# Kernel optimization log

Measured on AMD Instinct MI355X. Metric: run time of the kernel, lower is better.

The kernel has to match this reference:

```python
import jax, jax.numpy as jnp
import numpy as np

B = 8192
D_IN = 512
D_HID = 256
D_OUT = 128
EPS_STD = 1e-5
EPS_NORM = 1e-12


def _embed(x, W1, b1, W2, b2):
    # head: Linear -> ReLU -> Linear
    h = jax.nn.relu(x @ W1 + b1)          # (b, 256)
    y = h @ W2 + b2                        # (b, 128)
    # white(): per-feature batch whitening (center + unit std, unbiased like torch.std)
    mu = jnp.mean(y, axis=0, keepdims=True)
    sd = jnp.std(y, axis=0, keepdims=True, ddof=1) + EPS_STD
    y = (y - mu) / sd
    # F.normalize(p=2, dim=1)
    n = jnp.maximum(jnp.linalg.norm(y, axis=1, keepdims=True), EPS_NORM)
    return y / n


def _pair_loss(v1, v2):
    b = v1.shape[0]
    cat = jnp.concatenate([v1, v2], axis=0)            # (2b, d)
    inner = v1 @ cat.T                                  # (b, 2b) == broadcasted (v1*cat).sum(2)
    mask = jnp.concatenate(
        [1.0 - jnp.eye(b, dtype=inner.dtype), jnp.ones((b, b), dtype=inner.dtype)], axis=1)
    logits = inner * mask                               # zero out self-similarity logits
    logp = jax.nn.log_softmax(logits, axis=1)
    tgt = jnp.arange(b, 2 * b)                          # positive = matching row in v2 block
    return -jnp.take_along_axis(logp, tgt[:, None], axis=1).mean()


def setup_inputs() -> dict:
    key = jax.random.key(0)
    ks = jax.random.split(key, 16)
    def lin_init(k, fin, fout):
        bound = 1.0 / np.sqrt(fin)
        kw, kb = jax.random.split(k)
        W = jax.random.uniform(kw, (fin, fout), jnp.float32, -bound, bound)
        b = jax.random.uniform(kb, (fout,), jnp.float32, -bound, bound)
        return W, b
    inp = {
        'x_B': jax.random.normal(ks[0], (B, D_IN), jnp.float32),
        'x_E': jax.random.normal(ks[1], (B, D_IN), jnp.float32),
        'x_F': jax.random.normal(ks[2], (B, D_IN), jnp.float32),
    }
    for i, m in enumerate('BEF'):
        W1, b1 = lin_init(ks[3 + 2 * i], D_IN, D_HID)
        W2, b2 = lin_init(ks[4 + 2 * i], D_HID, D_OUT)
        inp[f'W1_{m}'] = W1; inp[f'b1_{m}'] = b1
        inp[f'W2_{m}'] = W2; inp[f'b2_{m}'] = b2
    return inp


def reference(x_B, x_E, x_F,
              W1_B, b1_B, W2_B, b2_B,
              W1_E, b1_E, W2_E, b2_E,
              W1_F, b1_F, W2_F, b2_F):
    zB = _embed(x_B, W1_B, b1_B, W2_B, b2_B)
    zE = _embed(x_E, W1_E, b1_E, W2_E, b2_E)
    zF = _embed(x_F, W1_F, b1_F, W2_F, b2_F)
    pairs = [(zB, zE), (zB, zF), (zE, zF)]  # itertools.combinations order
    loss = sum(_pair_loss(v1, v2) for v1, v2 in pairs) / len(pairs)
    return loss
```

## Files before the change

kernel.cpp:

```cpp
#include <hip/hip_runtime.h>
#include <hip/hip_bf16.h>
#include <math.h>

#define NROWS 8192
#define DIN   512
#define DHID  256
#define DOUT  128
#define LOG2E 1.4426950408889634f

typedef unsigned short ushort_t;
typedef __attribute__((ext_vector_type(8))) short bf16x8;
typedef __attribute__((ext_vector_type(4))) float f32x4;

#if defined(__has_builtin)
#  if __has_builtin(__builtin_amdgcn_exp2f)
#    define FAST_EXP2(x) __builtin_amdgcn_exp2f(x)
#  else
#    define FAST_EXP2(x) exp2f(x)
#  endif
#else
#  define FAST_EXP2(x) exp2f(x)
#endif

__device__ __forceinline__ short f2bf(float x) {
  __hip_bfloat16 h = __float2bfloat16(x);
  return *(short*)&h;
}

__device__ __forceinline__ bf16x8 cvt8(float4 lo, float4 hi) {
  bf16x8 r;
  r[0] = f2bf(lo.x); r[1] = f2bf(lo.y); r[2] = f2bf(lo.z); r[3] = f2bf(lo.w);
  r[4] = f2bf(hi.x); r[5] = f2bf(hi.y); r[6] = f2bf(hi.z); r[7] = f2bf(hi.w);
  return r;
}

__device__ __forceinline__ void dma16(const void* g, void* l) {
  __builtin_amdgcn_global_load_lds(
      (const __attribute__((address_space(1))) unsigned int*)g,
      (__attribute__((address_space(3))) unsigned int*)l, 16, 0, 0);
}

__global__ __launch_bounds__(256) void prep_w_kernel(
    const float* __restrict__ W1_0, const float* __restrict__ W1_1,
    const float* __restrict__ W1_2,
    const float* __restrict__ W2_0, const float* __restrict__ W2_1,
    const float* __restrict__ W2_2,
    ushort_t* __restrict__ w1t3, ushort_t* __restrict__ w2t3,
    float* __restrict__ zero_region)
{
  const int z = blockIdx.y;
  if (z == 0 && blockIdx.x < 163)
    zero_region[blockIdx.x * 256 + threadIdx.x] = 0.0f;
  const float* W1 = z == 0 ? W1_0 : (z == 1 ? W1_1 : W1_2);
  const float* W2 = z == 0 ? W2_0 : (z == 1 ? W2_1 : W2_2);
  int idx = blockIdx.x * 256 + threadIdx.x;
  if (idx < DHID * DIN) {
    int n = idx >> 9, k = idx & (DIN - 1);
    w1t3[(size_t)z * DHID * DIN + idx] = f2bf(W1[(size_t)k * DHID + n]);
  } else {
    int j = idx - DHID * DIN;
    int n = j >> 8, k = j & (DHID - 1);
    w2t3[(size_t)z * DOUT * DHID + j] = f2bf(W2[(size_t)k * DOUT + n]);
  }
}

#define MLP_BUF 20480
__global__ __launch_bounds__(256, 3) void mlp_kernel(
    const float* __restrict__ x0, const float* __restrict__ x1,
    const float* __restrict__ x2,
    const ushort_t* __restrict__ w1t3,
    const float* __restrict__ b1_0, const float* __restrict__ b1_1,
    const float* __restrict__ b1_2,
    const ushort_t* __restrict__ w2t3,
    const float* __restrict__ b2_0, const float* __restrict__ b2_1,
    const float* __restrict__ b2_2,
    float* __restrict__ y3,
    float* __restrict__ colsum, float* __restrict__ colsumsq)
{
  const int z = blockIdx.y;
  const float* X  = z == 0 ? x0 : (z == 1 ? x1 : x2);
  const float* B1 = z == 0 ? b1_0 : (z == 1 ? b1_1 : b1_2);
  const float* B2 = z == 0 ? b2_0 : (z == 1 ? b2_1 : b2_2);
  const ushort_t* W1t = w1t3 + (size_t)z * DHID * DIN;
  const ushort_t* W2t = w2t3 + (size_t)z * DOUT * DHID;
  float* Y    = y3 + (size_t)z * NROWS * DOUT;
  float* csum = colsum + z * DOUT;
  float* csq  = colsumsq + z * DOUT;

  __shared__ __align__(16) char lds[2 * MLP_BUF];
  ushort_t* hs = (ushort_t*)lds;

  const int tid = threadIdx.x, lane = tid & 63, wave = tid >> 6;
  const int quad = lane >> 4, l16 = lane & 15;
  const int m0 = blockIdx.x * 32;

  const char* w1b = (const char*)W1t;
  const char* wsrc[4];
#pragma unroll
  for (int jj = 0; jj < 4; jj++)
    wsrc[jj] = w1b + (size_t)(16 * (wave * 4 + jj) + l16) * 1024 +
               (lane >> 4) * 16;
  const int row8 = lane >> 3, slot = lane & 7;
  const int gseg = (slot + row8) & 7;
  const char* xsrc = (const char*)X +
      (size_t)(m0 + 8 * wave + row8) * 2048 + gseg * 16;

  f32x4 acc1[2][4] = {};
#pragma unroll
  for (int jj = 0; jj < 4; jj++)
    dma16(wsrc[jj], lds + (wave * 4 + jj) * 1024);
  dma16(xsrc, lds + 16384 + wave * 1024);
  __syncthreads();

  for (int c = 0; c < 16; c++) {
    const int buf = c & 1;
    if (c + 1 < 16) {
      char* dst = lds + (buf ^ 1) * MLP_BUF;
#pragma unroll
      for (int jj = 0; jj < 4; jj++)
        dma16(wsrc[jj] + (c + 1) * 64, dst + (wave * 4 + jj) * 1024);
      dma16(xsrc + (c + 1) * 128, dst + 16384 + wave * 1024);
    }
    const char* wb = lds + buf * MLP_BUF;
    const char* xb = wb + 16384;
    bf16x8 a[2];
#pragma unroll
    for (int mt = 0; mt < 2; mt++) {
      const int r = mt * 16 + l16, r7 = r & 7;
      const int s0 = (2 * quad - r7) & 7, s1 = (2 * quad + 1 - r7) & 7;
      float4 v0 = *(const float4*)(xb + r * 128 + s0 * 16);
      float4 v1 = *(const float4*)(xb + r * 128 + s1 * 16);
      a[mt] = cvt8(v0, v1);
    }
    bf16x8 b[4];
#pragma unroll
    for (int ct = 0; ct < 4; ct++)
      b[ct] = *(const bf16x8*)(wb + (wave * 4 + ct) * 1024 + quad * 256 +
                               l16 * 16);
#pragma unroll
    for (int mt = 0; mt < 2; mt++)
#pragma unroll
      for (int ct = 0; ct < 4; ct++)
        acc1[mt][ct] = __builtin_amdgcn_mfma_f32_16x16x32_bf16(
            a[mt], b[ct], acc1[mt][ct], 0, 0, 0);
    __syncthreads();
  }

  bf16x8 b2f[2][8];
#pragma unroll
  for (int ct = 0; ct < 2; ct++)
#pragma unroll
    for (int kk = 0; kk < 8; kk++)
      b2f[ct][kk] = *(const bf16x8*)(W2t +
          (size_t)(wave * 32 + ct * 16 + l16) * DHID + kk * 32 + quad * 8);

#pragma unroll
  for (int ct = 0; ct < 4; ct++) {
    float bb = B1[wave * 64 + ct * 16 + l16];
#pragma unroll
    for (int mt = 0; mt < 2; mt++)
#pragma unroll
      for (int reg = 0; reg < 4; reg++) {
        float v = fmaxf(acc1[mt][ct][reg] + bb, 0.0f);
        hs[(mt * 16 + quad * 4 + reg) * 264 + wave * 64 + ct * 16 + l16] =
            (ushort_t)f2bf(v);
      }
  }
  __syncthreads();

  f32x4 acc2[2][2] = {};
#pragma unroll
  for (int kk = 0; kk < 8; kk++) {
    bf16x8 a2[2];
#pragma unroll
    for (int mt = 0; mt < 2; mt++)
      a2[mt] = *(const bf16x8*)(hs + (mt * 16 + l16) * 264 + kk * 32 +
                                quad * 8);
#pragma unroll
    for (int mt = 0; mt < 2; mt++)
#pragma unroll
      for (int ct = 0; ct < 2; ct++)
        acc2[mt][ct] = __builtin_amdgcn_mfma_f32_16x16x32_bf16(
            a2[mt], b2f[ct][kk], acc2[mt][ct], 0, 0, 0);
  }

#pragma unroll
  for (int ct = 0; ct < 2; ct++) {
    const int colo = wave * 32 + ct * 16 + l16;
    float bb = B2[colo];
    float cs = 0.0f, cq = 0.0f;
#pragma unroll
    for (int mt = 0; mt < 2; mt++)
#pragma unroll
      for (int reg = 0; reg < 4; reg++) {
        float v = acc2[mt][ct][reg] + bb;
        Y[(size_t)(m0 + mt * 16 + quad * 4 + reg) * DOUT + colo] = v;
        cs += v; cq += v * v;
      }
    cs += __shfl_xor(cs, 16, 64); cs += __shfl_xor(cs, 32, 64);
    cq += __shfl_xor(cq, 16, 64); cq += __shfl_xor(cq, 32, 64);
    if (lane < 16) {
      atomicAdd(&csum[colo], cs);
      atomicAdd(&csq[colo], cq);
    }
  }
}

__global__ __launch_bounds__(256) void whiten_kernel(
    const float* __restrict__ y3,
    const float* __restrict__ colsum, const float* __restrict__ colsumsq,
    ushort_t* __restrict__ zB, ushort_t* __restrict__ zE,
    ushort_t* __restrict__ zF,
    ushort_t* __restrict__ zBs, ushort_t* __restrict__ zEs,
    float* __restrict__ pos)
{
  const int tid = threadIdx.x, lane = tid & 63, wave = tid >> 6;
  const int row = blockIdx.x * 4 + wave;
  const size_t base = (size_t)row * DOUT;
  const size_t hsz = (size_t)NROWS * DOUT;
  const int c0 = lane, c1 = lane + 64;

  float mu[3][2], isd[3][2];
#pragma unroll
  for (int h = 0; h < 3; h++) {
#pragma unroll
    for (int cc = 0; cc < 2; cc++) {
      const int idx = h * DOUT + (cc ? c1 : c0);
      float m = colsum[idx] * (1.0f / NROWS);
      float var = (colsumsq[idx] - (float)NROWS * m * m) *
                  (1.0f / (NROWS - 1));
      mu[h][cc] = m;
      isd[h][cc] = 1.0f / (sqrtf(fmaxf(var, 0.0f)) + 1e-5f);
    }
  }

  float vB0 = (y3[base + c0]           - mu[0][0]) * isd[0][0];
  float vB1 = (y3[base + c1]           - mu[0][1]) * isd[0][1];
  float vE0 = (y3[base + hsz + c0]     - mu[1][0]) * isd[1][0];
  float vE1 = (y3[base + hsz + c1]     - mu[1][1]) * isd[1][1];
  float vF0 = (y3[base + 2 * hsz + c0] - mu[2][0]) * isd[2][0];
  float vF1 = (y3[base + 2 * hsz + c1] - mu[2][1]) * isd[2][1];

  float nB = vB0 * vB0 + vB1 * vB1;
  float nE = vE0 * vE0 + vE1 * vE1;
  float nF = vF0 * vF0 + vF1 * vF1;
#pragma unroll
  for (int o = 1; o < 64; o <<= 1) {
    nB += __shfl_xor(nB, o, 64);
    nE += __shfl_xor(nE, o, 64);
    nF += __shfl_xor(nF, o, 64);
  }
  float iB = 1.0f / fmaxf(sqrtf(nB), 1e-12f);
  float iE = 1.0f / fmaxf(sqrtf(nE), 1e-12f);
  float iF = 1.0f / fmaxf(sqrtf(nF), 1e-12f);
  float zb0 = vB0 * iB, zb1 = vB1 * iB;
  float ze0 = vE0 * iE, ze1 = vE1 * iE;
  float zf0 = vF0 * iF, zf1 = vF1 * iF;

  zB[base + c0]  = (ushort_t)f2bf(zb0);
  zB[base + c1]  = (ushort_t)f2bf(zb1);
  zE[base + c0]  = (ushort_t)f2bf(ze0);
  zE[base + c1]  = (ushort_t)f2bf(ze1);
  zF[base + c0]  = (ushort_t)f2bf(zf0);
  zF[base + c1]  = (ushort_t)f2bf(zf1);
  zBs[base + c0] = (ushort_t)f2bf(zb0 * LOG2E);
  zBs[base + c1] = (ushort_t)f2bf(zb1 * LOG2E);
  zEs[base + c0] = (ushort_t)f2bf(ze0 * LOG2E);
  zEs[base + c1] = (ushort_t)f2bf(ze1 * LOG2E);

  float pBE = zb0 * ze0 + zb1 * ze1;
  float pBF = zb0 * zf0 + zb1 * zf1;
  float pEF = ze0 * zf0 + ze1 * zf1;
#pragma unroll
  for (int o = 1; o < 64; o <<= 1) {
    pBE += __shfl_xor(pBE, o, 64);
    pBF += __shfl_xor(pBF, o, 64);
    pEF += __shfl_xor(pEF, o, 64);
  }
  if (lane == 0) {
    pos[row]             = pBE;
    pos[NROWS + row]     = pBF;
    pos[2 * NROWS + row] = pEF;
  }
}

#define G_CH  32
#define G_NCH 32
__global__ __launch_bounds__(256, 3) void gram_kernel(
    const ushort_t* __restrict__ zB, const ushort_t* __restrict__ zE,
    const ushort_t* __restrict__ zF,
    const ushort_t* __restrict__ zBs, const ushort_t* __restrict__ zEs,
    float* __restrict__ rowsum)
{
  const ushort_t *U, *V;
  float* rs;
  switch (blockIdx.z) {
    case 0:  U = zBs; V = zB; rs = rowsum;             break;
    case 1:  U = zEs; V = zE; rs = rowsum + NROWS;     break;
    case 2:  U = zBs; V = zE; rs = rowsum + 2 * NROWS; break;
    case 3:  U = zBs; V = zF; rs = rowsum + 3 * NROWS; break;
    default: U = zEs; V = zF; rs = rowsum + 4 * NROWS; break;
  }

  const int tid = threadIdx.x, lane = tid & 63, wave = tid >> 6;
  const int quad = lane >> 4, l16 = lane & 15;
  const int m0 = blockIdx.x * 256 + wave * 64;
  const int col0 = blockIdx.y * (G_CH * G_NCH);

  __shared__ __align__(16) ushort_t sbuf[2][4096];

  const ushort_t* ua = U + (size_t)(m0 + l16) * DOUT + quad * 8;
  bf16x8 a[4][4];
#pragma unroll
  for (int rt = 0; rt < 4; rt++)
#pragma unroll
    for (int ki = 0; ki < 4; ki++)
      a[rt][ki] = *(const bf16x8*)(ua + rt * 16 * DOUT + ki * 32);

  const char* Vb = (const char*)V;
  const int r_ = lane & 31, hi_ = lane >> 5;
  const int s0 = 4 * wave + hi_, s1 = 4 * wave + 2 + hi_;
  const char* g0 = Vb + (size_t)(col0 + r_) * 256 + (s0 >> 2) * 64 + (s0 & 3) * 16;
  const char* g1 = Vb + (size_t)(col0 + r_) * 256 + (s1 >> 2) * 64 + (s1 & 3) * 16;

  float rsum[4][4] = {};
  const f32x4 zero = {0.0f, 0.0f, 0.0f, 0.0f};

  dma16(g0, &sbuf[0][(2 * wave) * 512]);
  dma16(g1, &sbuf[0][(2 * wave + 1) * 512]);
  __syncthreads();

  for (int c = 0; c < G_NCH; c++) {
    const int buf = c & 1;
    if (c + 1 < G_NCH) {
      const size_t go = (size_t)(c + 1) * 8192;
      dma16(g0 + go, &sbuf[buf ^ 1][(2 * wave) * 512]);
      dma16(g1 + go, &sbuf[buf ^ 1][(2 * wave + 1) * 512]);
    }
    const char* sb = (const char*)&sbuf[buf][0];
    bf16x8 b[4][2];
#pragma unroll
    for (int ki = 0; ki < 4; ki++)
#pragma unroll
      for (int ct = 0; ct < 2; ct++)
        b[ki][ct] = *(const bf16x8*)(sb + (ki * 4 + quad) * 512 +
                                     (ct * 16 + l16) * 16);
    f32x4 acc[4][2];
#pragma unroll
    for (int ki = 0; ki < 4; ki++)
#pragma unroll
      for (int rt = 0; rt < 4; rt++)
#pragma unroll
        for (int ct = 0; ct < 2; ct++)
          acc[rt][ct] = __builtin_amdgcn_mfma_f32_16x16x32_bf16(
              a[rt][ki], b[ki][ct], ki == 0 ? zero : acc[rt][ct], 0, 0, 0);
#pragma unroll
    for (int rt = 0; rt < 4; rt++)
#pragma unroll
      for (int reg = 0; reg < 4; reg++)
        rsum[rt][reg] += FAST_EXP2(acc[rt][0][reg]) + FAST_EXP2(acc[rt][1][reg]);
    __syncthreads();
  }

#pragma unroll
  for (int rt = 0; rt < 4; rt++)
#pragma unroll
    for (int reg = 0; reg < 4; reg++) {
      float s = rsum[rt][reg];
      s += __shfl_xor(s, 1, 64);
      s += __shfl_xor(s, 2, 64);
      s += __shfl_xor(s, 4, 64);
      s += __shfl_xor(s, 8, 64);
      if (l16 == 0)
        atomicAdd(&rs[m0 + rt * 16 + quad * 4 + reg], s);
    }
}

__global__ __launch_bounds__(1024) void loss_kernel(
    const float* __restrict__ rowsum, const float* __restrict__ pos,
    float* __restrict__ out)
{
  const float* sB  = rowsum;
  const float* sE  = rowsum + NROWS;
  const float* cBE = rowsum + 2 * NROWS;
  const float* cBF = rowsum + 3 * NROWS;
  const float* cEF = rowsum + 4 * NROWS;
  const float* pBE = pos;
  const float* pBF = pos + NROWS;
  const float* pEF = pos + 2 * NROWS;

  const float corr = 1.0f - expf(1.0f);
  float local = 0.0f;
  for (int i = threadIdx.x; i < NROWS; i += 1024) {
    float selB = sB[i] + corr;
    float selE = sE[i] + corr;
    local += __logf(selB + cBE[i]) - pBE[i];
    local += __logf(selB + cBF[i]) - pBF[i];
    local += __logf(selE + cEF[i]) - pEF[i];
  }
  __shared__ float red[16];
#pragma unroll
  for (int o = 32; o > 0; o >>= 1) local += __shfl_down(local, o, 64);
  int lane = threadIdx.x & 63, wv = threadIdx.x >> 6;
  if (lane == 0) red[wv] = local;
  __syncthreads();
  if (threadIdx.x == 0) {
    float t = 0.0f;
#pragma unroll
    for (int w = 0; w < 16; w++) t += red[w];
    out[0] = t / (3.0f * (float)NROWS);
  }
}

extern "C" void kernel_launch(void* const* d_in, const int* in_sizes, int n_in,
                              void* d_out, int out_size, void* d_ws, size_t ws_size,
                              hipStream_t stream)
{
  const float* xs[3] = {(const float*)d_in[0], (const float*)d_in[1], (const float*)d_in[2]};
  const float* W1[3] = {(const float*)d_in[3], (const float*)d_in[7],  (const float*)d_in[11]};
  const float* b1[3] = {(const float*)d_in[4], (const float*)d_in[8],  (const float*)d_in[12]};
  const float* W2[3] = {(const float*)d_in[5], (const float*)d_in[9],  (const float*)d_in[13]};
  const float* b2[3] = {(const float*)d_in[6], (const float*)d_in[10], (const float*)d_in[14]};

  float* ws = (float*)d_ws;
  float* colsum   = ws;
  float* colsumsq = ws + 384;
  float* rowsum   = ws + 768;
  float* pos      = ws + 42496;
  ushort_t* w1t3 = (ushort_t*)(ws + 67072);
  ushort_t* w2t3 = (ushort_t*)(ws + 263680);
  float*    y3   = ws + 312832;
  ushort_t* zB   = (ushort_t*)(ws + 3458560);
  ushort_t* zE   = zB  + (size_t)NROWS * DOUT;
  ushort_t* zF   = zE  + (size_t)NROWS * DOUT;
  ushort_t* zBs  = zF  + (size_t)NROWS * DOUT;
  ushort_t* zEs  = zBs + (size_t)NROWS * DOUT;

  prep_w_kernel<<<dim3(640, 3), 256, 0, stream>>>(
      W1[0], W1[1], W1[2], W2[0], W2[1], W2[2], w1t3, w2t3, ws);
  mlp_kernel<<<dim3(256, 3), 256, 0, stream>>>(
      xs[0], xs[1], xs[2], w1t3, b1[0], b1[1], b1[2],
      w2t3, b2[0], b2[1], b2[2], y3, colsum, colsumsq);
  whiten_kernel<<<2048, 256, 0, stream>>>(
      y3, colsum, colsumsq, zB, zE, zF, zBs, zEs, pos);
  gram_kernel<<<dim3(32, 8, 5), 256, 0, stream>>>(zB, zE, zF, zBs, zEs, rowsum);
  loss_kernel<<<1, 1024, 0, stream>>>(rowsum, pos, (float*)d_out);
}
```

Baseline: 233.4 us.

## Enlarge MLP row tile, store pre-whitening output in bf16, tile weight transpose, parallelize loss

The MLP kernel now handles 64 rows per block instead of 32, so each staged W1 chunk is reused across twice as many rows. Occupancy drops to 2 blocks per CU and the grid halves. The intermediate y buffer is stored as bf16 rather than fp32, which halves that write/read traffic into the whitening kernel at some precision cost. The weight-prep transpose now goes through an LDS tile so both reads and writes are coalesced, and it also zeroes the output. The single-block loss reduction is replaced by 32 blocks that atomically accumulate into the output.

```diff
diff --git a/kernel.cpp b/kernel.cpp
--- a/kernel.cpp
+++ b/kernel.cpp
@@ -27,6 +27,12 @@
   return *(short*)&h;
 }
 
+__device__ __forceinline__ float bf2f(ushort_t v) {
+  unsigned int u = ((unsigned int)v) << 16;
+  union { unsigned int u; float f; } c; c.u = u;
+  return c.f;
+}
+
 __device__ __forceinline__ bf16x8 cvt8(float4 lo, float4 hi) {
   bf16x8 r;
   r[0] = f2bf(lo.x); r[1] = f2bf(lo.y); r[2] = f2bf(lo.z); r[3] = f2bf(lo.w);
@@ -46,26 +52,57 @@
     const float* __restrict__ W2_0, const float* __restrict__ W2_1,
     const float* __restrict__ W2_2,
     ushort_t* __restrict__ w1t3, ushort_t* __restrict__ w2t3,
-    float* __restrict__ zero_region)
-{
-  const int z = blockIdx.y;
-  if (z == 0 && blockIdx.x < 163)
-    zero_region[blockIdx.x * 256 + threadIdx.x] = 0.0f;
+    float* __restrict__ zero_region, float* __restrict__ out)
+{
+  const int z = blockIdx.z, gx = blockIdx.x, gy = blockIdx.y;
+  const int tid = threadIdx.x;
+  if (z == 0) {
+    int b = gy * 4 + gx;
+#pragma unroll
+    for (int j = 0; j < 4; j++) {
+      int idx = b * 256 + tid + j * 12288;
+      if (idx < 41728) zero_region[idx] = 0.0f;
+    }
+    if (b == 0 && tid == 0) out[0] = 0.0f;
+  }
   const float* W1 = z == 0 ? W1_0 : (z == 1 ? W1_1 : W1_2);
   const float* W2 = z == 0 ? W2_0 : (z == 1 ? W2_1 : W2_2);
-  int idx = blockIdx.x * 256 + threadIdx.x;
-  if (idx < DHID * DIN) {
-    int n = idx >> 9, k = idx & (DIN - 1);
-    w1t3[(size_t)z * DHID * DIN + idx] = f2bf(W1[(size_t)k * DHID + n]);
+
+  __shared__ float t[64][65];
+  if (gy < 8) {
+    const int k0 = gy * 64, n0 = gx * 64;
+#pragma unroll
+    for (int it = 0; it < 16; it++) {
+      int r = it * 4 + (tid >> 6), c = tid & 63;
+      t[r][c] = W1[(size_t)(k0 + r) * DHID + n0 + c];
+    }
+    __syncthreads();
+    ushort_t* dst = w1t3 + (size_t)z * DHID * DIN;
+#pragma unroll
+    for (int it = 0; it < 16; it++) {
+      int n = it * 4 + (tid >> 6), k = tid & 63;
+      dst[(size_t)(n0 + n) * DIN + k0 + k] = (ushort_t)f2bf(t[k][n]);
+    }
   } else {
-    int j = idx - DHID * DIN;
-    int n = j >> 8, k = j & (DHID - 1);
-    w2t3[(size_t)z * DOUT * DHID + j] = f2bf(W2[(size_t)k * DOUT + n]);
-  }
-}
-
-#define MLP_BUF 20480
-__global__ __launch_bounds__(256, 3) void mlp_kernel(
+    if (gx >= 2) return;
+    const int k0 = (gy - 8) * 64, n0 = gx * 64;
+#pragma unroll
+    for (int it = 0; it < 16; it++) {
+      int r = it * 4 + (tid >> 6), c = tid & 63;
+      t[r][c] = W2[(size_t)(k0 + r) * DOUT + n0 + c];
+    }
+    __syncthreads();
+    ushort_t* dst = w2t3 + (size_t)z * DOUT * DHID;
+#pragma unroll
+    for (int it = 0; it < 16; it++) {
+      int n = it * 4 + (tid >> 6), k = tid & 63;
+      dst[(size_t)(n0 + n) * DHID + k0 + k] = (ushort_t)f2bf(t[k][n]);
+    }
+  }
+}
+
+#define MLP_BUF 24576
+__global__ __launch_bounds__(256, 2) void mlp_kernel(
     const float* __restrict__ x0, const float* __restrict__ x1,
     const float* __restrict__ x2,
     const ushort_t* __restrict__ w1t3,
@@ -74,7 +111,7 @@
     const ushort_t* __restrict__ w2t3,
     const float* __restrict__ b2_0, const float* __restrict__ b2_1,
     const float* __restrict__ b2_2,
-    float* __restrict__ y3,
+    ushort_t* __restrict__ y3,
     float* __restrict__ colsum, float* __restrict__ colsumsq)
 {
   const int z = blockIdx.y;
@@ -83,7 +120,7 @@
   const float* B2 = z == 0 ? b2_0 : (z == 1 ? b2_1 : b2_2);
   const ushort_t* W1t = w1t3 + (size_t)z * DHID * DIN;
   const ushort_t* W2t = w2t3 + (size_t)z * DOUT * DHID;
-  float* Y    = y3 + (size_t)z * NROWS * DOUT;
+  ushort_t* Y = y3 + (size_t)z * NROWS * DOUT;
   float* csum = colsum + z * DOUT;
   float* csq  = colsumsq + z * DOUT;
 
@@ -92,24 +129,28 @@
 
   const int tid = threadIdx.x, lane = tid & 63, wave = tid >> 6;
   const int quad = lane >> 4, l16 = lane & 15;
-  const int m0 = blockIdx.x * 32;
+  const int m0 = blockIdx.x * 64;
 
   const char* w1b = (const char*)W1t;
   const char* wsrc[4];
 #pragma unroll
   for (int jj = 0; jj < 4; jj++)
-    wsrc[jj] = w1b + (size_t)(16 * (wave * 4 + jj) + l16) * 1024 +
-               (lane >> 4) * 16;
+    wsrc[jj] = w1b + (size_t)(16 * (wave * 4 + jj) + l16) * 1024 + quad * 16;
   const int row8 = lane >> 3, slot = lane & 7;
   const int gseg = (slot + row8) & 7;
-  const char* xsrc = (const char*)X +
-      (size_t)(m0 + 8 * wave + row8) * 2048 + gseg * 16;
-
-  f32x4 acc1[2][4] = {};
+  const char* xsrc[2];
+#pragma unroll
+  for (int jj = 0; jj < 2; jj++)
+    xsrc[jj] = (const char*)X +
+        (size_t)(m0 + 8 * (wave * 2 + jj) + row8) * 2048 + gseg * 16;
+
+  f32x4 acc1[4][4] = {};
 #pragma unroll
   for (int jj = 0; jj < 4; jj++)
     dma16(wsrc[jj], lds + (wave * 4 + jj) * 1024);
-  dma16(xsrc, lds + 16384 + wave * 1024);
+#pragma unroll
+  for (int jj = 0; jj < 2; jj++)
+    dma16(xsrc[jj], lds + 16384 + (wave * 2 + jj) * 1024);
   __syncthreads();
 
   for (int c = 0; c < 16; c++) {
@@ -119,13 +160,15 @@
 #pragma unroll
       for (int jj = 0; jj < 4; jj++)
         dma16(wsrc[jj] + (c + 1) * 64, dst + (wave * 4 + jj) * 1024);
-      dma16(xsrc + (c + 1) * 128, dst + 16384 + wave * 1024);
+#pragma unroll
+      for (int jj = 0; jj < 2; jj++)
+        dma16(xsrc[jj] + (c + 1) * 128, dst + 16384 + (wave * 2 + jj) * 1024);
     }
     const char* wb = lds + buf * MLP_BUF;
     const char* xb = wb + 16384;
-    bf16x8 a[2];
-#pragma unroll
-    for (int mt = 0; mt < 2; mt++) {
+    bf16x8 a[4];
+#pragma unroll
+    for (int mt = 0; mt < 4; mt++) {
       const int r = mt * 16 + l16, r7 = r & 7;
       const int s0 = (2 * quad - r7) & 7, s1 = (2 * quad + 1 - r7) & 7;
       float4 v0 = *(const float4*)(xb + r * 128 + s0 * 16);
@@ -138,7 +181,7 @@
       b[ct] = *(const bf16x8*)(wb + (wave * 4 + ct) * 1024 + quad * 256 +
                                l16 * 16);
 #pragma unroll
-    for (int mt = 0; mt < 2; mt++)
+    for (int mt = 0; mt < 4; mt++)
 #pragma unroll
       for (int ct = 0; ct < 4; ct++)
         acc1[mt][ct] = __builtin_amdgcn_mfma_f32_16x16x32_bf16(
@@ -158,7 +201,7 @@
   for (int ct = 0; ct < 4; ct++) {
     float bb = B1[wave * 64 + ct * 16 + l16];
 #pragma unroll
-    for (int mt = 0; mt < 2; mt++)
+    for (int mt = 0; mt < 4; mt++)
 #pragma unroll
       for (int reg = 0; reg < 4; reg++) {
         float v = fmaxf(acc1[mt][ct][reg] + bb, 0.0f);
@@ -168,16 +211,16 @@
   }
   __syncthreads();
 
-  f32x4 acc2[2][2] = {};
+  f32x4 acc2[4][2] = {};
 #pragma unroll
   for (int kk = 0; kk < 8; kk++) {
-    bf16x8 a2[2];
-#pragma unroll
-    for (int mt = 0; mt < 2; mt++)
+    bf16x8 a2[4];
+#pragma unroll
+    for (int mt = 0; mt < 4; mt++)
       a2[mt] = *(const bf16x8*)(hs + (mt * 16 + l16) * 264 + kk * 32 +
                                 quad * 8);
 #pragma unroll
-    for (int mt = 0; mt < 2; mt++)
+    for (int mt = 0; mt < 4; mt++)
 #pragma unroll
       for (int ct = 0; ct < 2; ct++)
         acc2[mt][ct] = __builtin_amdgcn_mfma_f32_16x16x32_bf16(
@@ -190,11 +233,12 @@
     float bb = B2[colo];
     float cs = 0.0f, cq = 0.0f;
 #pragma unroll
-    for (int mt = 0; mt < 2; mt++)
+    for (int mt = 0; mt < 4; mt++)
 #pragma unroll
       for (int reg = 0; reg < 4; reg++) {
         float v = acc2[mt][ct][reg] + bb;
-        Y[(size_t)(m0 + mt * 16 + quad * 4 + reg) * DOUT + colo] = v;
+        Y[(size_t)(m0 + mt * 16 + quad * 4 + reg) * DOUT + colo] =
+            (ushort_t)f2bf(v);
         cs += v; cq += v * v;
       }
     cs += __shfl_xor(cs, 16, 64); cs += __shfl_xor(cs, 32, 64);
@@ -207,7 +251,7 @@
 }
 
 __global__ __launch_bounds__(256) void whiten_kernel(
-    const float* __restrict__ y3,
+    const ushort_t* __restrict__ y3,
     const float* __restrict__ colsum, const float* __restrict__ colsumsq,
     ushort_t* __restrict__ zB, ushort_t* __restrict__ zE,
     ushort_t* __restrict__ zF,
@@ -234,12 +278,12 @@
     }
   }
 
-  float vB0 = (y3[base + c0]           - mu[0][0]) * isd[0][0];
-  float vB1 = (y3[base + c1]           - mu[0][1]) * isd[0][1];
-  float vE0 = (y3[base + hsz + c0]     - mu[1][0]) * isd[1][0];
-  float vE1 = (y3[base + hsz + c1]     - mu[1][1]) * isd[1][1];
-  float vF0 = (y3[base + 2 * hsz + c0] - mu[2][0]) * isd[2][0];
-  float vF1 = (y3[base + 2 * hsz + c1] - mu[2][1]) * isd[2][1];
+  float vB0 = (bf2f(y3[base + c0])           - mu[0][0]) * isd[0][0];
+  float vB1 = (bf2f(y3[base + c1])           - mu[0][1]) * isd[0][1];
+  float vE0 = (bf2f(y3[base + hsz + c0])     - mu[1][0]) * isd[1][0];
+  float vE1 = (bf2f(y3[base + hsz + c1])     - mu[1][1]) * isd[1][1];
+  float vF0 = (bf2f(y3[base + 2 * hsz + c0]) - mu[2][0]) * isd[2][0];
+  float vF1 = (bf2f(y3[base + 2 * hsz + c1]) - mu[2][1]) * isd[2][1];
 
   float nB = vB0 * vB0 + vB1 * vB1;
   float nE = vE0 * vE0 + vE1 * vE1;
@@ -376,7 +420,7 @@
     }
 }
 
-__global__ __launch_bounds__(1024) void loss_kernel(
+__global__ __launch_bounds__(256) void loss_kernel(
     const float* __restrict__ rowsum, const float* __restrict__ pos,
     float* __restrict__ out)
 {
@@ -389,26 +433,23 @@
   const float* pBF = pos + NROWS;
   const float* pEF = pos + 2 * NROWS;
 
+  const int i = blockIdx.x * 256 + threadIdx.x;
   const float corr = 1.0f - expf(1.0f);
-  float local = 0.0f;
-  for (int i = threadIdx.x; i < NROWS; i += 1024) {
-    float selB = sB[i] + corr;
-    float selE = sE[i] + corr;
-    local += __logf(selB + cBE[i]) - pBE[i];
-    local += __logf(selB + cBF[i]) - pBF[i];
-    local += __logf(selE + cEF[i]) - pEF[i];
-  }
-  __shared__ float red[16];
+  float selB = sB[i] + corr;
+  float selE = sE[i] + corr;
+  float local = __logf(selB + cBE[i]) - pBE[i];
+  local += __logf(selB + cBF[i]) - pBF[i];
+  local += __logf(selE + cEF[i]) - pEF[i];
+
+  __shared__ float red[4];
 #pragma unroll
   for (int o = 32; o > 0; o >>= 1) local += __shfl_down(local, o, 64);
   int lane = threadIdx.x & 63, wv = threadIdx.x >> 6;
   if (lane == 0) red[wv] = local;
   __syncthreads();
   if (threadIdx.x == 0) {
-    float t = 0.0f;
-#pragma unroll
-    for (int w = 0; w < 16; w++) t += red[w];
-    out[0] = t / (3.0f * (float)NROWS);
+    float t = red[0] + red[1] + red[2] + red[3];
+    atomicAdd(out, t * (1.0f / (3.0f * (float)NROWS)));
   }
 }
 
@@ -429,20 +470,20 @@
   float* pos      = ws + 42496;
   ushort_t* w1t3 = (ushort_t*)(ws + 67072);
   ushort_t* w2t3 = (ushort_t*)(ws + 263680);
-  float*    y3   = ws + 312832;
-  ushort_t* zB   = (ushort_t*)(ws + 3458560);
+  ushort_t* y3b  = (ushort_t*)(ws + 312832);
+  ushort_t* zB   = (ushort_t*)(ws + 1885696);
   ushort_t* zE   = zB  + (size_t)NROWS * DOUT;
   ushort_t* zF   = zE  + (size_t)NROWS * DOUT;
   ushort_t* zBs  = zF  + (size_t)NROWS * DOUT;
   ushort_t* zEs  = zBs + (size_t)NROWS * DOUT;
 
-  prep_w_kernel<<<dim3(640, 3), 256, 0, stream>>>(
-      W1[0], W1[1], W1[2], W2[0], W2[1], W2[2], w1t3, w2t3, ws);
-  mlp_kernel<<<dim3(256, 3), 256, 0, stream>>>(
+  prep_w_kernel<<<dim3(4, 12, 3), 256, 0, stream>>>(
+      W1[0], W1[1], W1[2], W2[0], W2[1], W2[2], w1t3, w2t3, ws, (float*)d_out);
+  mlp_kernel<<<dim3(128, 3), 256, 0, stream>>>(
       xs[0], xs[1], xs[2], w1t3, b1[0], b1[1], b1[2],
-      w2t3, b2[0], b2[1], b2[2], y3, colsum, colsumsq);
+      w2t3, b2[0], b2[1], b2[2], y3b, colsum, colsumsq);
   whiten_kernel<<<2048, 256, 0, stream>>>(
-      y3, colsum, colsumsq, zB, zE, zF, zBs, zEs, pos);
+      y3b, colsum, colsumsq, zB, zE, zF, zBs, zEs, pos);
   gram_kernel<<<dim3(32, 8, 5), 256, 0, stream>>>(zB, zE, zF, zBs, zEs, rowsum);
-  loss_kernel<<<1, 1024, 0, stream>>>(rowsum, pos, (float*)d_out);
-}
+  loss_kernel<<<32, 256, 0, stream>>>(rowsum, pos, (float*)d_out);
+}
```

Result: faster. 219.3 us (median of 3 runs) (-6.0%).
